# Kernel tuning notes

Hardware: AMD Instinct MI355X
Metric: run time of the kernel (lower is better)

Reference implementation:

```python
import jax, jax.numpy as jnp
import numpy as np
import math

D_MODEL = 512
N_HEADS = 8
FACTOR = 5
B, L = 2, 2048


def setup_inputs() -> dict:
    key = jax.random.key(0)
    ks = jax.random.split(key, 10)
    s = 1.0 / math.sqrt(D_MODEL)
    inp = {
        "x": jax.random.normal(ks[0], (B, L, D_MODEL), dtype=jnp.float32),
        "samp_idx": jax.random.randint(ks[1], (FACTOR * L,), 0, L),
        "Wq": jax.random.normal(ks[2], (D_MODEL, D_MODEL), dtype=jnp.float32) * s,
        "bq": jnp.zeros((D_MODEL,), dtype=jnp.float32),
        "Wk": jax.random.normal(ks[3], (D_MODEL, D_MODEL), dtype=jnp.float32) * s,
        "bk": jnp.zeros((D_MODEL,), dtype=jnp.float32),
        "Wv": jax.random.normal(ks[4], (D_MODEL, D_MODEL), dtype=jnp.float32) * s,
        "bv": jnp.zeros((D_MODEL,), dtype=jnp.float32),
        "Wo": jax.random.normal(ks[5], (D_MODEL, D_MODEL), dtype=jnp.float32) * s,
        "bo": jnp.zeros((D_MODEL,), dtype=jnp.float32),
    }
    return inp


def reference(x, Wq, bq, Wk, bk, Wv, bv, Wo, bo, samp_idx):
    B_, L_, D = x.shape
    H = N_HEADS
    dk = D // H
    scale = 1.0 / math.sqrt(dk)

    def proj(W, b):
        # torch Linear: x @ W.T + b, then split heads -> [B, H, L, dk]
        y = jnp.einsum('bld,ed->ble', x, W) + b
        return y.reshape(B_, L_, H, dk).transpose(0, 2, 1, 3)

    q = proj(Wq, bq)
    k = proj(Wk, bk)
    v = proj(Wv, bv)

    # _prob_QK: random key sampling (shared indices across B, H)
    K_sample = k[:, :, samp_idx, :]                       # [B, H, factor*L, dk]
    QKs = jnp.einsum('bhle,bhse->bhls', q, K_sample) * scale  # [B, H, L, factor*L]
    M = QKs.max(-1) - QKs.mean(-1)                        # [B, H, L]
    U = jnp.argmax(M, axis=-1)                            # [B, H] -- single query per head

    # gather the selected query per (b, h): [B, H, 1, dk]
    q_red = jnp.take_along_axis(q, U[:, :, None, None], axis=2)

    scores = jnp.einsum('bhle,bhse->bhls', q_red, k) * scale  # [B, H, 1, L]
    attn = jax.nn.softmax(scores, axis=-1)
    context = jnp.einsum('bhls,bhse->bhle', attn, v)          # [B, H, 1, dk]

    # expand to all query positions, merge heads
    context = jnp.broadcast_to(context, (B_, H, L_, dk))
    context = context.transpose(0, 2, 1, 3).reshape(B_, L_, D)
    return jnp.einsum('bld,ed->ble', context, Wo) + bo
```

## Files before the change

### kernel.cpp

```cpp
#include <hip/hip_runtime.h>

#define B_ 2
#define L_ 2048
#define D_ 512
#define H_ 8
#define DK 64
#define S_ 10240
#define SCALE 0.125f

#define QSZ (4096 * 512)

typedef _Float16 f16;
typedef __attribute__((ext_vector_type(8))) _Float16 f16x8;
typedef __attribute__((ext_vector_type(4))) float f32x4;

#define AS1 __attribute__((address_space(1)))
#define AS3 __attribute__((address_space(3)))

__global__ __launch_bounds__(256) void prep_kernel(
    const float* __restrict__ x,
    const float* __restrict__ Wq, const float* __restrict__ Wk,
    const float* __restrict__ bq, const float* __restrict__ bk,
    const int* __restrict__ samp,
    f16* __restrict__ xh, f16* __restrict__ xl,
    f16* __restrict__ wh, f16* __restrict__ wl,
    float* __restrict__ biascat, int* __restrict__ counts,
    float* __restrict__ xbc_part)
{
    const int bid = blockIdx.x;
    const int t = threadIdx.x;
    if (bid < 1024) {
        const size_t i0 = ((size_t)bid * 256 + t) * 8;
        const float4 a = *(const float4*)&x[i0];
        const float4 b = *(const float4*)&x[i0 + 4];
        const float vals[8] = {a.x, a.y, a.z, a.w, b.x, b.y, b.z, b.w};
        union { f16 h[8]; uint4 u; } H, Lo;
#pragma unroll
        for (int j = 0; j < 8; j++) {
            const f16 hh = (f16)vals[j];
            H.h[j] = hh;
            Lo.h[j] = (f16)(vals[j] - (float)hh);
        }
        *(uint4*)&xh[i0] = H.u;
        *(uint4*)&xl[i0] = Lo.u;
    } else if (bid < 1280) {
        const size_t i0 = ((size_t)(bid - 1024) * 256 + t) * 8;
        const float* src = (i0 < (size_t)512 * 512) ? Wq + i0
                                                    : Wk + (i0 - (size_t)512 * 512);
        const float4 a = *(const float4*)&src[0];
        const float4 b = *(const float4*)&src[4];
        const float vals[8] = {a.x, a.y, a.z, a.w, b.x, b.y, b.z, b.w};
        union { f16 h[8]; uint4 u; } H, Lo;
#pragma unroll
        for (int j = 0; j < 8; j++) {
            const f16 hh = (f16)vals[j];
            H.h[j] = hh;
            Lo.h[j] = (f16)(vals[j] - (float)hh);
        }
        *(uint4*)&wh[i0] = H.u;
        *(uint4*)&wl[i0] = Lo.u;
        if (bid == 1024)
            for (int e = t; e < 1024; e += 256)
                biascat[e] = (e < 512) ? bq[e] : bk[e - 512];
    } else if (bid < 1344) {
        const int p = bid - 1280;
        const int bb = p >> 5, chunk = p & 31;
        const int s0 = chunk * 320;
        float ax = 0.f, ay = 0.f;
        const float* xb = x + (size_t)bb * L_ * D_ + t * 2;
        for (int i = 0; i < 320; i++) {
            const int j = samp[s0 + i];
            const float2 v = *(const float2*)(xb + (size_t)j * D_);
            ax += v.x; ay += v.y;
        }
        float2 st; st.x = ax; st.y = ay;
        *(float2*)&xbc_part[((size_t)(bb * 32 + chunk)) * 512 + t * 2] = st;
    } else {
        int4 z; z.x = 0; z.y = 0; z.z = 0; z.w = 0;
        ((int4*)counts)[(bid - 1344) * 256 + t] = z;
    }
}

__global__ __launch_bounds__(256) void projqk_kernel(
    const f16* __restrict__ xh, const f16* __restrict__ xl,
    const f16* __restrict__ wh, const f16* __restrict__ wl,
    const float* __restrict__ biascat,
    const float* __restrict__ xbc_part, const float* __restrict__ Wk,
    const float* __restrict__ bk, const int* __restrict__ samp,
    int* __restrict__ counts, float* __restrict__ kbar,
    f16* __restrict__ qh, f16* __restrict__ ql,
    f16* __restrict__ kh, f16* __restrict__ kl)
{
    const int bid = blockIdx.x;
    const int t = threadIdx.x;

    __shared__ __align__(16) f16 lds[4 * 128 * 64];

    if (bid >= 256) {
        const int bh = bid - 256;
        const int b = bh >> 3, h = bh & 7;
        float* xc = (float*)lds;

        for (int i = bh * 640 + t; i < (bh + 1) * 640; i += 256)
            atomicAdd(&counts[samp[i]], 1);

        float ax = 0.f, ay = 0.f;
#pragma unroll
        for (int p = 0; p < 32; p++) {
            const float2 v = *(const float2*)&xbc_part[((size_t)(b * 32 + p)) * 512 + t * 2];
            ax += v.x; ay += v.y;
        }
        xc[t * 2]     = ax * (1.0f / (float)S_);
        xc[t * 2 + 1] = ay * (1.0f / (float)S_);
        __syncthreads();

        const int row = t >> 2, quarter = t & 3;
        const float* wr = Wk + (size_t)(h * 64 + row) * 512 + quarter * 128;
        float s = 0.f;
#pragma unroll 8
        for (int d = 0; d < 32; d++) {
            const float4 w4 = *(const float4*)&wr[d * 4];
            const int xo = quarter * 128 + d * 4;
            s += w4.x * xc[xo] + w4.y * xc[xo + 1] + w4.z * xc[xo + 2] + w4.w * xc[xo + 3];
        }
        s += __shfl_xor(s, 1);
        s += __shfl_xor(s, 2);
        if (quarter == 0) kbar[bh * 64 + row] = s + bk[h * 64 + row];
        return;
    }

    const int n0 = (bid & 31) * 128;
    const int e0 = (bid >> 5) * 128;

    f16* ash = lds;
    f16* asl = lds + 8192;
    f16* bsh = lds + 16384;
    f16* bsl = lds + 24576;

    const int lane = t & 63, wid = t >> 6;
    const int wr = wid >> 1, wc = wid & 1;
    const int lrow = lane & 15, lk = lane >> 4;
    const int srw = lane >> 3;
    const int scg = (lane & 7) ^ srw;

    f32x4 acc[4][4];
#pragma unroll
    for (int i = 0; i < 4; i++)
#pragma unroll
        for (int j = 0; j < 4; j++)
#pragma unroll
            for (int r = 0; r < 4; r++) acc[i][j][r] = 0.f;

    for (int kt = 0; kt < 8; kt++) {
        __syncthreads();
#pragma unroll
        for (int i_ = 0; i_ < 4; i_++) {
            const int chunk = wid * 4 + i_;
            const int row = chunk * 8 + srw;
            const size_t goa = (size_t)(n0 + row) * 512 + kt * 64 + scg * 8;
            const size_t gob = (size_t)(e0 + row) * 512 + kt * 64 + scg * 8;
            __builtin_amdgcn_global_load_lds((const AS1 void*)(xh + goa),
                                             (AS3 void*)(&ash[chunk * 512]), 16, 0, 0);
            __builtin_amdgcn_global_load_lds((const AS1 void*)(xl + goa),
                                             (AS3 void*)(&asl[chunk * 512]), 16, 0, 0);
            __builtin_amdgcn_global_load_lds((const AS1 void*)(wh + gob),
                                             (AS3 void*)(&bsh[chunk * 512]), 16, 0, 0);
            __builtin_amdgcn_global_load_lds((const AS1 void*)(wl + gob),
                                             (AS3 void*)(&bsl[chunk * 512]), 16, 0, 0);
        }
        __syncthreads();

#pragma unroll
        for (int kk = 0; kk < 2; kk++) {
            f16x8 ah[4], al[4], bh_[4], bl_[4];
#pragma unroll
            for (int lt = 0; lt < 4; lt++) {
                const int row = wr * 64 + lt * 16 + lrow;
                const int cs = (kk * 4 + lk) ^ (row & 7);
                const int o = row * 64 + cs * 8;
                ah[lt] = *(const f16x8*)&ash[o];
                al[lt] = *(const f16x8*)&asl[o];
            }
#pragma unroll
            for (int jt = 0; jt < 4; jt++) {
                const int row = wc * 64 + jt * 16 + lrow;
                const int cs = (kk * 4 + lk) ^ (row & 7);
                const int o = row * 64 + cs * 8;
                bh_[jt] = *(const f16x8*)&bsh[o];
                bl_[jt] = *(const f16x8*)&bsl[o];
            }
#pragma unroll
            for (int lt = 0; lt < 4; lt++)
#pragma unroll
                for (int jt = 0; jt < 4; jt++) {
                    acc[lt][jt] = __builtin_amdgcn_mfma_f32_16x16x32_f16(
                        ah[lt], bh_[jt], acc[lt][jt], 0, 0, 0);
                    acc[lt][jt] = __builtin_amdgcn_mfma_f32_16x16x32_f16(
                        ah[lt], bl_[jt], acc[lt][jt], 0, 0, 0);
                    acc[lt][jt] = __builtin_amdgcn_mfma_f32_16x16x32_f16(
                        al[lt], bh_[jt], acc[lt][jt], 0, 0, 0);
                }
        }
    }

    const int PSTR = 72;
    f16* tile = lds + wid * 64 * PSTR;
    const int ebase = e0 + wc * 64;
    const bool isQ = ((bid >> 5) < 4);
    const int colbase = ((bid >> 5) & 3) * 128;

#pragma unroll
    for (int round = 0; round < 2; round++) {
        __syncthreads();
#pragma unroll
        for (int jt = 0; jt < 4; jt++) {
            const float bval = biascat[ebase + jt * 16 + lrow];
#pragma unroll
            for (int lt = 0; lt < 4; lt++)
#pragma unroll
                for (int r = 0; r < 4; r++) {
                    const float y = acc[lt][jt][r] + bval;
                    const f16 hi = (f16)y;
                    const f16 val = (round == 0) ? hi : (f16)(y - (float)hi);
                    tile[(lt * 16 + lk * 4 + r) * PSTR + jt * 16 + lrow] = val;
                }
        }
        __syncthreads();
        f16* dst = isQ ? ((round == 0) ? qh : ql) : ((round == 0) ? kh : kl);
        for (int i = t; i < 2048; i += 256) {
            const int w = i >> 9, rem = i & 511, row = rem >> 3, c = rem & 7;
            const int n = n0 + (w >> 1) * 64 + row;
            const int col = colbase + (w & 1) * 64 + c * 8;
            *(uint4*)&dst[(size_t)n * 512 + col] =
                *(const uint4*)&lds[w * 64 * PSTR + row * PSTR + c * 8];
        }
    }
}

__global__ __launch_bounds__(256, 2) void mstat_kernel(
    const f16* __restrict__ qh, const f16* __restrict__ ql,
    const f16* __restrict__ kh, const f16* __restrict__ kl,
    const int* __restrict__ counts, const float* __restrict__ kbar,
    float* __restrict__ bestv, int* __restrict__ besti)
{
    const int id = blockIdx.x;
    const int xcd = id & 7, seq = id >> 3;
    const int bh = xcd * 2 + (seq >> 5);
    const int inner = seq & 31;
    const int lt16 = inner >> 1;
    const int js = inner & 1;
    const int jbase = js * 8;
    const int b = bh >> 3, h = bh & 7;
    const int l0 = lt16 * 128;
    const int t = threadIdx.x;
    const int lane = t & 63, wid = t >> 6;
    const int wr = wid >> 1, wc = wid & 1;
    const int lrow = lane & 15, lk = lane >> 4;

    __shared__ __align__(16) f16 kbuf[2][2][128 * 64];
    __shared__ float kbar_lds[64];
    __shared__ float dot_lds[128];
    __shared__ float wv_[4];
    __shared__ int wi_[4];

    f16x8 qa_h[2][4], qa_l[2][4];
    {
        const size_t qrowbase = (size_t)(b * L_ + l0 + wr * 64) * D_ + h * DK;
#pragma unroll
        for (int kk = 0; kk < 2; kk++)
#pragma unroll
            for (int lt = 0; lt < 4; lt++) {
                const size_t o = qrowbase + (size_t)(lt * 16 + lrow) * D_ + kk * 32 + lk * 8;
                qa_h[kk][lt] = *(const f16x8*)&qh[o];
                qa_l[kk][lt] = *(const f16x8*)&ql[o];
            }
    }
    if (t < 64) kbar_lds[t] = kbar[bh * 64 + t];

    const f16* khb = kh + (size_t)b * L_ * D_ + h * DK;
    const f16* klb = kl + (size_t)b * L_ * D_ + h * DK;

    const int srw = lane >> 3;
    const int scg = (lane & 7) ^ srw;
#define STAGE_TILE(jt, nb)                                                     \
    {                                                                          \
        const size_t gb0 = (size_t)((jt) * 128) * D_;                          \
        _Pragma("unroll")                                                      \
        for (int i_ = 0; i_ < 4; i_++) {                                       \
            const int chunk = wid * 4 + i_;                                    \
            const size_t go = gb0 + (size_t)(chunk * 8 + srw) * D_ + scg * 8;  \
            __builtin_amdgcn_global_load_lds(                                  \
                (const AS1 void*)(khb + go),                                   \
                (AS3 void*)(&kbuf[nb][0][chunk * 512]), 16, 0, 0);             \
            __builtin_amdgcn_global_load_lds(                                  \
                (const AS1 void*)(klb + go),                                   \
                (AS3 void*)(&kbuf[nb][1][chunk * 512]), 16, 0, 0);             \
        }                                                                      \
    }

    STAGE_TILE(jbase, 0)
    __syncthreads();

    float rmax[4][4];
#pragma unroll
    for (int lt = 0; lt < 4; lt++)
#pragma unroll
        for (int r = 0; r < 4; r++) rmax[lt][r] = -3.9e38f;

    int cur = 0;
    for (int jj = 0; jj < 8; jj++) {
        const int jt = jbase + jj;
        if (jj < 7) STAGE_TILE(jt + 1, cur ^ 1)

        f32x4 acc[4][4];
#pragma unroll
        for (int i = 0; i < 4; i++)
#pragma unroll
            for (int j = 0; j < 4; j++)
#pragma unroll
                for (int r = 0; r < 4; r++) acc[i][j][r] = 0.f;

#pragma unroll
        for (int kk = 0; kk < 2; kk++) {
            f16x8 bhf[4], blf[4];
#pragma unroll
            for (int jtt = 0; jtt < 4; jtt++) {
                const int row = wc * 64 + jtt * 16 + lrow;
                const int cs = (kk * 4 + lk) ^ (row & 7);
                const int o = row * 64 + cs * 8;
                bhf[jtt] = *(const f16x8*)&kbuf[cur][0][o];
                blf[jtt] = *(const f16x8*)&kbuf[cur][1][o];
            }
#pragma unroll
            for (int lt = 0; lt < 4; lt++)
#pragma unroll
                for (int jtt = 0; jtt < 4; jtt++) {
                    acc[lt][jtt] = __builtin_amdgcn_mfma_f32_16x16x32_f16(
                        qa_h[kk][lt], bhf[jtt], acc[lt][jtt], 0, 0, 0);
                    acc[lt][jtt] = __builtin_amdgcn_mfma_f32_16x16x32_f16(
                        qa_h[kk][lt], blf[jtt], acc[lt][jtt], 0, 0, 0);
                    acc[lt][jtt] = __builtin_amdgcn_mfma_f32_16x16x32_f16(
                        qa_l[kk][lt], bhf[jtt], acc[lt][jtt], 0, 0, 0);
                }
        }

#pragma unroll
        for (int jtt = 0; jtt < 4; jtt++) {
            const int cj = jt * 128 + wc * 64 + jtt * 16 + lrow;
            const float addend = (counts[cj] > 0) ? 0.f : -3.0e38f;
#pragma unroll
            for (int lt = 0; lt < 4; lt++)
#pragma unroll
                for (int r = 0; r < 4; r++)
                    rmax[lt][r] = fmaxf(rmax[lt][r], acc[lt][jtt][r] + addend);
        }

        __syncthreads();
        cur ^= 1;
    }

#pragma unroll
    for (int m = 1; m < 16; m <<= 1)
#pragma unroll
        for (int lt = 0; lt < 4; lt++)
#pragma unroll
            for (int r = 0; r < 4; r++)
                rmax[lt][r] = fmaxf(rmax[lt][r], __shfl_xor(rmax[lt][r], m));

    {
        float dlt[4];
#pragma unroll
        for (int lt = 0; lt < 4; lt++) {
            float d = 0.f;
#pragma unroll
            for (int kk = 0; kk < 2; kk++) {
                const f16x8 hv = qa_h[kk][lt];
                const f16x8 lv = qa_l[kk][lt];
#pragma unroll
                for (int i = 0; i < 8; i++)
                    d += ((float)hv[i] + (float)lv[i]) * kbar_lds[kk * 32 + lk * 8 + i];
            }
            dlt[lt] = d;
        }
#pragma unroll
        for (int lt = 0; lt < 4; lt++) {
            dlt[lt] += __shfl_xor(dlt[lt], 16);
            dlt[lt] += __shfl_xor(dlt[lt], 32);
        }
        if (lane < 16) {
#pragma unroll
            for (int lt = 0; lt < 4; lt++)
                dot_lds[wr * 64 + lt * 16 + lane] = dlt[lt];
        }
    }
    __syncthreads();

    float bv_ = -3.9e38f;
    int bi_ = 0x7fffffff;
#pragma unroll
    for (int lt = 0; lt < 4; lt++)
#pragma unroll
        for (int r = 0; r < 4; r++) {
            const int rl_ = wr * 64 + lt * 16 + lk * 4 + r;
            const float val = rmax[lt][r] - dot_lds[rl_];
            const int idx = l0 + rl_;
            if (val > bv_ || (val == bv_ && idx < bi_)) { bv_ = val; bi_ = idx; }
        }
#pragma unroll
    for (int m = 1; m < 64; m <<= 1) {
        const float ov = __shfl_xor(bv_, m);
        const int oi = __shfl_xor(bi_, m);
        if (ov > bv_ || (ov == bv_ && oi < bi_)) { bv_ = ov; bi_ = oi; }
    }
    if (lane == 0) { wv_[wid] = bv_; wi_[wid] = bi_; }
    __syncthreads();
    if (t == 0) {
        float fb = wv_[0]; int fi = wi_[0];
#pragma unroll
        for (int w = 1; w < 4; w++) {
            if (wv_[w] > fb || (wv_[w] == fb && wi_[w] < fi)) { fb = wv_[w]; fi = wi_[w]; }
        }
        bestv[bh * 32 + lt16 * 2 + js] = fb;
        besti[bh * 32 + lt16 * 2 + js] = fi;
    }
#undef STAGE_TILE
}

__global__ __launch_bounds__(256) void ctx_part_kernel(
    const f16* __restrict__ qh, const f16* __restrict__ ql,
    const f16* __restrict__ kh, const f16* __restrict__ kl,
    const float* __restrict__ x,
    const float* __restrict__ bestv, const int* __restrict__ besti,
    float* __restrict__ xbar_part, float* __restrict__ cm, float* __restrict__ cs)
{
    const int c = blockIdx.x;
    const int b = blockIdx.y;
    const int l0 = c * 16;
    const int t = threadIdx.x;

    __shared__ float qr[8][64];
    __shared__ float w[8][16];
    __shared__ int u_lds[8];

    if (t < 8) {
        const int bh = b * 8 + t;
        float best = -3.9e38f; int bi = 0x7fffffff;
        for (int cc = 0; cc < 32; cc++) {
            const float v = bestv[bh * 32 + cc];
            const int oi = besti[bh * 32 + cc];
            if (v > best || (v == best && oi < bi)) { best = v; bi = oi; }
        }
        u_lds[t] = bi;
    }
    __syncthreads();

    {
        const int h = t >> 5, i2 = (t & 31) * 2;
        const int u = u_lds[h];
        const size_t o = (size_t)(b * L_ + u) * D_ + h * DK + i2;
        qr[h][i2]     = (float)qh[o]     + (float)ql[o];
        qr[h][i2 + 1] = (float)qh[o + 1] + (float)ql[o + 1];
    }
    __syncthreads();

    {
        const int dotid = t >> 1, half = t & 1;
        const int row = dotid & 15, h = dotid >> 4;
        const size_t off = (size_t)(b * L_ + l0 + row) * D_ + h * DK + half * 32;
        const f16* krh = kh + off;
        const f16* krl = kl + off;
        float dot = 0.f;
#pragma unroll
        for (int cc = 0; cc < 4; cc++) {
            const f16x8 hv = *(const f16x8*)&krh[cc * 8];
            const f16x8 lv = *(const f16x8*)&krl[cc * 8];
#pragma unroll
            for (int i = 0; i < 8; i++)
                dot += ((float)hv[i] + (float)lv[i]) * qr[h][half * 32 + cc * 8 + i];
        }
        dot += __shfl_xor(dot, 1);
        if (half == 0) w[h][row] = dot * SCALE;
    }
    __syncthreads();

    if (t < 8) {
        float m = w[t][0];
#pragma unroll
        for (int i = 1; i < 16; i++) m = fmaxf(m, w[t][i]);
        float s = 0.f;
#pragma unroll
        for (int i = 0; i < 16; i++) {
            const float e = expf(w[t][i] - m);
            w[t][i] = e;
            s += e;
        }
        cm[(size_t)(b * 8 + t) * 128 + c] = m;
        cs[(size_t)(b * 8 + t) * 128 + c] = s;
    }
    __syncthreads();

    {
        float ax[8], ay[8];
#pragma unroll
        for (int h = 0; h < 8; h++) { ax[h] = 0.f; ay[h] = 0.f; }
        const float* xb = x + (size_t)(b * L_ + l0) * D_ + t * 2;
#pragma unroll
        for (int i = 0; i < 16; i++) {
            const float2 xv = *(const float2*)(xb + (size_t)i * D_);
#pragma unroll
            for (int h = 0; h < 8; h++) {
                ax[h] = fmaf(w[h][i], xv.x, ax[h]);
                ay[h] = fmaf(w[h][i], xv.y, ay[h]);
            }
        }
#pragma unroll
        for (int h = 0; h < 8; h++) {
            float2 st; st.x = ax[h]; st.y = ay[h];
            *(float2*)&xbar_part[((size_t)(b * 8 + h) * 128 + c) * 512 + t * 2] = st;
        }
    }
}

__global__ __launch_bounds__(256) void ctx_combine_kernel(
    const float* __restrict__ xbar_part, const float* __restrict__ cm,
    const float* __restrict__ cs, const float* __restrict__ Wv,
    const float* __restrict__ bv, float* __restrict__ ctx)
{
    const int bh = blockIdx.x;
    const int h = bh & 7;
    const int t = threadIdx.x;
    __shared__ float xbar[512];

    float M = -3.9e38f;
    for (int cc = 0; cc < 128; cc++) M = fmaxf(M, cm[(size_t)bh * 128 + cc]);
    float denom = 0.f, ax = 0.f, ay = 0.f;
    for (int cc = 0; cc < 128; cc++) {
        const float f = expf(cm[(size_t)bh * 128 + cc] - M);
        denom += f * cs[(size_t)bh * 128 + cc];
        const float2 p = *(const float2*)
            &xbar_part[((size_t)bh * 128 + cc) * 512 + t * 2];
        ax = fmaf(f, p.x, ax);
        ay = fmaf(f, p.y, ay);
    }
    xbar[t * 2] = ax; xbar[t * 2 + 1] = ay;
    __syncthreads();

    if (t < 64) {
        const float* wr = Wv + (size_t)(h * 64 + t) * D_;
        float acc = 0.f;
#pragma unroll 8
        for (int d = 0; d < 128; d++) {
            const float4 wv4 = *(const float4*)&wr[d * 4];
            acc += wv4.x * xbar[d * 4] + wv4.y * xbar[d * 4 + 1] +
                   wv4.z * xbar[d * 4 + 2] + wv4.w * xbar[d * 4 + 3];
        }
        ctx[bh * 64 + t] = acc / denom + bv[h * 64 + t];
    }
}

__global__ __launch_bounds__(256) void out_kernel(
    const float* __restrict__ ctx, const float* __restrict__ Wo,
    const float* __restrict__ bo, float* __restrict__ out)
{
    const int b = blockIdx.x;
    const int sl = blockIdx.y;
    const int t = threadIdx.x;
    __shared__ float cb[512];
    __shared__ float row[512];

    cb[t] = ctx[b * 512 + t];
    cb[t + 256] = ctx[b * 512 + 256 + t];
    __syncthreads();

#pragma unroll
    for (int r = 0; r < 2; r++) {
        const int e = t + r * 256;
        const float* wr = Wo + (size_t)e * D_;
        float acc = 0.f;
#pragma unroll 8
        for (int c = 0; c < 128; c++) {
            const float4 wv = *(const float4*)(wr + c * 4);
            acc += wv.x * cb[c * 4] + wv.y * cb[c * 4 + 1] +
                   wv.z * cb[c * 4 + 2] + wv.w * cb[c * 4 + 3];
        }
        row[e] = acc + bo[e];
    }
    __syncthreads();

    const float4* r4 = (const float4*)row;
    float4* o4 = (float4*)(out + ((size_t)b * L_ + sl * 32) * D_);
    for (int i = t; i < 32 * 128; i += 256) {
        const int l = i >> 7, c = i & 127;
        o4[l * 128 + c] = r4[c];
    }
}

extern "C" void kernel_launch(void* const* d_in, const int* in_sizes, int n_in,
                              void* d_out, int out_size, void* d_ws, size_t ws_size,
                              hipStream_t stream)
{
    const float* x   = (const float*)d_in[0];
    const int* samp  = (const int*)d_in[1];
    const float* Wq  = (const float*)d_in[2];
    const float* bq  = (const float*)d_in[3];
    const float* Wk  = (const float*)d_in[4];
    const float* bk  = (const float*)d_in[5];
    const float* Wv  = (const float*)d_in[6];
    const float* bv  = (const float*)d_in[7];
    const float* Wo  = (const float*)d_in[8];
    const float* bo  = (const float*)d_in[9];
    float* out = (float*)d_out;

    f16* qh = (f16*)d_ws;
    f16* ql = qh + QSZ;
    f16* kh = ql + QSZ;
    f16* kl = kh + QSZ;
    f16* xh = kl + QSZ;
    f16* xl = xh + QSZ;
    f16* wh = xl + QSZ;
    f16* wl = wh + 1024 * 512;
    float* fbase     = (float*)(wl + 1024 * 512);
    float* biascat   = fbase;
    float* xbc_part  = biascat + 1024;
    float* xbar_part = xbc_part + 32768;
    float* cm        = xbar_part + 1048576;
    float* cs        = cm + 2048;
    float* bestv     = cs + 2048;
    float* kbar      = bestv + 512;
    float* ctx       = kbar + 1024;
    int* counts      = (int*)(ctx + 1024);
    int* besti       = counts + 2048;

    prep_kernel<<<1346, 256, 0, stream>>>(x, Wq, Wk, bq, bk, samp,
                                          xh, xl, wh, wl, biascat, counts,
                                          xbc_part);
    projqk_kernel<<<272, 256, 0, stream>>>(xh, xl, wh, wl, biascat,
                                           xbc_part, Wk, bk, samp, counts, kbar,
                                           qh, ql, kh, kl);
    mstat_kernel<<<512, 256, 0, stream>>>(qh, ql, kh, kl, counts, kbar,
                                          bestv, besti);
    ctx_part_kernel<<<dim3(128, 2), 256, 0, stream>>>(qh, ql, kh, kl, x,
                                                      bestv, besti,
                                                      xbar_part, cm, cs);
    ctx_combine_kernel<<<16, 256, 0, stream>>>(xbar_part, cm, cs, Wv, bv, ctx);
    out_kernel<<<dim3(2, 64), 256, 0, stream>>>(ctx, Wo, bo, out);
}
```

Baseline: 145.0 us.

## Fuse ctx_part, ctx_combine and out kernels into one flag-synchronized tail kernel

```diff
diff --git a/kernel.cpp b/kernel.cpp
--- a/kernel.cpp
+++ b/kernel.cpp
@@ -25,7 +25,7 @@
     f16* __restrict__ xh, f16* __restrict__ xl,
     f16* __restrict__ wh, f16* __restrict__ wl,
     float* __restrict__ biascat, int* __restrict__ counts,
-    float* __restrict__ xbc_part)
+    float* __restrict__ xbc_part, int* __restrict__ flags)
 {
     const int bid = blockIdx.x;
     const int t = threadIdx.x;
@@ -78,6 +78,7 @@
     } else {
         int4 z; z.x = 0; z.y = 0; z.z = 0; z.w = 0;
         ((int4*)counts)[(bid - 1344) * 256 + t] = z;
+        if (bid == 1344 && t == 0) { flags[0] = 0; flags[1] = 0; }
     }
 }
 
@@ -426,172 +427,194 @@
 #undef STAGE_TILE
 }
 
-__global__ __launch_bounds__(256) void ctx_part_kernel(
+__global__ __launch_bounds__(256) void tail_kernel(
     const f16* __restrict__ qh, const f16* __restrict__ ql,
     const f16* __restrict__ kh, const f16* __restrict__ kl,
     const float* __restrict__ x,
     const float* __restrict__ bestv, const int* __restrict__ besti,
-    float* __restrict__ xbar_part, float* __restrict__ cm, float* __restrict__ cs)
+    const float* __restrict__ Wv, const float* __restrict__ bv,
+    const float* __restrict__ Wo, const float* __restrict__ bo,
+    float* __restrict__ xbar_part, float* __restrict__ cm,
+    float* __restrict__ cs, float* __restrict__ ctx,
+    float* __restrict__ out, int* __restrict__ flags)
 {
-    const int c = blockIdx.x;
-    const int b = blockIdx.y;
-    const int l0 = c * 16;
+    const int bid = blockIdx.x;
     const int t = threadIdx.x;
 
-    __shared__ float qr[8][64];
-    __shared__ float w[8][16];
-    __shared__ int u_lds[8];
-
-    if (t < 8) {
-        const int bh = b * 8 + t;
-        float best = -3.9e38f; int bi = 0x7fffffff;
-        for (int cc = 0; cc < 32; cc++) {
-            const float v = bestv[bh * 32 + cc];
-            const int oi = besti[bh * 32 + cc];
-            if (v > best || (v == best && oi < bi)) { best = v; bi = oi; }
-        }
-        u_lds[t] = bi;
-    }
-    __syncthreads();
-
-    {
-        const int h = t >> 5, i2 = (t & 31) * 2;
-        const int u = u_lds[h];
-        const size_t o = (size_t)(b * L_ + u) * D_ + h * DK + i2;
-        qr[h][i2]     = (float)qh[o]     + (float)ql[o];
-        qr[h][i2 + 1] = (float)qh[o + 1] + (float)ql[o + 1];
-    }
-    __syncthreads();
-
-    {
-        const int dotid = t >> 1, half = t & 1;
-        const int row = dotid & 15, h = dotid >> 4;
-        const size_t off = (size_t)(b * L_ + l0 + row) * D_ + h * DK + half * 32;
-        const f16* krh = kh + off;
-        const f16* krl = kl + off;
-        float dot = 0.f;
-#pragma unroll
-        for (int cc = 0; cc < 4; cc++) {
-            const f16x8 hv = *(const f16x8*)&krh[cc * 8];
-            const f16x8 lv = *(const f16x8*)&krl[cc * 8];
-#pragma unroll
-            for (int i = 0; i < 8; i++)
-                dot += ((float)hv[i] + (float)lv[i]) * qr[h][half * 32 + cc * 8 + i];
-        }
-        dot += __shfl_xor(dot, 1);
-        if (half == 0) w[h][row] = dot * SCALE;
-    }
-    __syncthreads();
-
-    if (t < 8) {
-        float m = w[t][0];
-#pragma unroll
-        for (int i = 1; i < 16; i++) m = fmaxf(m, w[t][i]);
-        float s = 0.f;
-#pragma unroll
-        for (int i = 0; i < 16; i++) {
-            const float e = expf(w[t][i] - m);
-            w[t][i] = e;
-            s += e;
-        }
-        cm[(size_t)(b * 8 + t) * 128 + c] = m;
-        cs[(size_t)(b * 8 + t) * 128 + c] = s;
-    }
-    __syncthreads();
-
-    {
-        float ax[8], ay[8];
-#pragma unroll
-        for (int h = 0; h < 8; h++) { ax[h] = 0.f; ay[h] = 0.f; }
-        const float* xb = x + (size_t)(b * L_ + l0) * D_ + t * 2;
-#pragma unroll
-        for (int i = 0; i < 16; i++) {
-            const float2 xv = *(const float2*)(xb + (size_t)i * D_);
+    if (bid < 256) {
+        const int c = bid & 127;
+        const int b = bid >> 7;
+        const int l0 = c * 16;
+
+        __shared__ float qr[8][64];
+        __shared__ float w[8][16];
+        __shared__ int u_lds[8];
+
+        if (t < 8) {
+            const int bh = b * 8 + t;
+            float best = -3.9e38f; int bi = 0x7fffffff;
+            for (int cc = 0; cc < 32; cc++) {
+                const float v = bestv[bh * 32 + cc];
+                const int oi = besti[bh * 32 + cc];
+                if (v > best || (v == best && oi < bi)) { best = v; bi = oi; }
+            }
+            u_lds[t] = bi;
+        }
+        __syncthreads();
+
+        {
+            const int h = t >> 5, i2 = (t & 31) * 2;
+            const int u = u_lds[h];
+            const size_t o = (size_t)(b * L_ + u) * D_ + h * DK + i2;
+            qr[h][i2]     = (float)qh[o]     + (float)ql[o];
+            qr[h][i2 + 1] = (float)qh[o + 1] + (float)ql[o + 1];
+        }
+        __syncthreads();
+
+        {
+            const int dotid = t >> 1, half = t & 1;
+            const int row = dotid & 15, h = dotid >> 4;
+            const size_t off = (size_t)(b * L_ + l0 + row) * D_ + h * DK + half * 32;
+            const f16* krh = kh + off;
+            const f16* krl = kl + off;
+            float dot = 0.f;
+#pragma unroll
+            for (int cc = 0; cc < 4; cc++) {
+                const f16x8 hv = *(const f16x8*)&krh[cc * 8];
+                const f16x8 lv = *(const f16x8*)&krl[cc * 8];
+#pragma unroll
+                for (int i = 0; i < 8; i++)
+                    dot += ((float)hv[i] + (float)lv[i]) * qr[h][half * 32 + cc * 8 + i];
+            }
+            dot += __shfl_xor(dot, 1);
+            if (half == 0) w[h][row] = dot * SCALE;
+        }
+        __syncthreads();
+
+        if (t < 8) {
+            float m = w[t][0];
+#pragma unroll
+            for (int i = 1; i < 16; i++) m = fmaxf(m, w[t][i]);
+            float s = 0.f;
+#pragma unroll
+            for (int i = 0; i < 16; i++) {
+                const float e = expf(w[t][i] - m);
+                w[t][i] = e;
+                s += e;
+            }
+            cm[(size_t)(b * 8 + t) * 128 + c] = m;
+            cs[(size_t)(b * 8 + t) * 128 + c] = s;
+        }
+        __syncthreads();
+
+        {
+            float ax[8], ay[8];
+#pragma unroll
+            for (int h = 0; h < 8; h++) { ax[h] = 0.f; ay[h] = 0.f; }
+            const float* xb = x + (size_t)(b * L_ + l0) * D_ + t * 2;
+#pragma unroll
+            for (int i = 0; i < 16; i++) {
+                const float2 xv = *(const float2*)(xb + (size_t)i * D_);
+#pragma unroll
+                for (int h = 0; h < 8; h++) {
+                    ax[h] = fmaf(w[h][i], xv.x, ax[h]);
+                    ay[h] = fmaf(w[h][i], xv.y, ay[h]);
+                }
+            }
 #pragma unroll
             for (int h = 0; h < 8; h++) {
-                ax[h] = fmaf(w[h][i], xv.x, ax[h]);
-                ay[h] = fmaf(w[h][i], xv.y, ay[h]);
-            }
-        }
-#pragma unroll
-        for (int h = 0; h < 8; h++) {
-            float2 st; st.x = ax[h]; st.y = ay[h];
-            *(float2*)&xbar_part[((size_t)(b * 8 + h) * 128 + c) * 512 + t * 2] = st;
-        }
-    }
-}
-
-__global__ __launch_bounds__(256) void ctx_combine_kernel(
-    const float* __restrict__ xbar_part, const float* __restrict__ cm,
-    const float* __restrict__ cs, const float* __restrict__ Wv,
-    const float* __restrict__ bv, float* __restrict__ ctx)
-{
-    const int bh = blockIdx.x;
-    const int h = bh & 7;
-    const int t = threadIdx.x;
-    __shared__ float xbar[512];
-
-    float M = -3.9e38f;
-    for (int cc = 0; cc < 128; cc++) M = fmaxf(M, cm[(size_t)bh * 128 + cc]);
-    float denom = 0.f, ax = 0.f, ay = 0.f;
-    for (int cc = 0; cc < 128; cc++) {
-        const float f = expf(cm[(size_t)bh * 128 + cc] - M);
-        denom += f * cs[(size_t)bh * 128 + cc];
-        const float2 p = *(const float2*)
-            &xbar_part[((size_t)bh * 128 + cc) * 512 + t * 2];
-        ax = fmaf(f, p.x, ax);
-        ay = fmaf(f, p.y, ay);
-    }
-    xbar[t * 2] = ax; xbar[t * 2 + 1] = ay;
-    __syncthreads();
-
-    if (t < 64) {
-        const float* wr = Wv + (size_t)(h * 64 + t) * D_;
-        float acc = 0.f;
+                float2 st; st.x = ax[h]; st.y = ay[h];
+                *(float2*)&xbar_part[((size_t)(b * 8 + h) * 128 + c) * 512 + t * 2] = st;
+            }
+        }
+
+        __threadfence();
+        __syncthreads();
+        if (t == 0)
+            __hip_atomic_fetch_add(&flags[0], 1, __ATOMIC_RELEASE,
+                                   __HIP_MEMORY_SCOPE_AGENT);
+    } else if (bid < 272) {
+        const int bh = bid - 256;
+        const int h = bh & 7;
+        __shared__ float xbar[512];
+
+        if (t == 0) {
+            while (__hip_atomic_load(&flags[0], __ATOMIC_ACQUIRE,
+                                     __HIP_MEMORY_SCOPE_AGENT) < 256)
+                __builtin_amdgcn_s_sleep(8);
+        }
+        __syncthreads();
+
+        float M = -3.9e38f;
+        for (int cc = 0; cc < 128; cc++) M = fmaxf(M, cm[(size_t)bh * 128 + cc]);
+        float denom = 0.f, ax = 0.f, ay = 0.f;
+        for (int cc = 0; cc < 128; cc++) {
+            const float f = expf(cm[(size_t)bh * 128 + cc] - M);
+            denom += f * cs[(size_t)bh * 128 + cc];
+            const float2 p = *(const float2*)
+                &xbar_part[((size_t)bh * 128 + cc) * 512 + t * 2];
+            ax = fmaf(f, p.x, ax);
+            ay = fmaf(f, p.y, ay);
+        }
+        xbar[t * 2] = ax; xbar[t * 2 + 1] = ay;
+        __syncthreads();
+
+        if (t < 64) {
+            const float* wr = Wv + (size_t)(h * 64 + t) * D_;
+            float acc = 0.f;
 #pragma unroll 8
-        for (int d = 0; d < 128; d++) {
-            const float4 wv4 = *(const float4*)&wr[d * 4];
-            acc += wv4.x * xbar[d * 4] + wv4.y * xbar[d * 4 + 1] +
-                   wv4.z * xbar[d * 4 + 2] + wv4.w * xbar[d * 4 + 3];
-        }
-        ctx[bh * 64 + t] = acc / denom + bv[h * 64 + t];
-    }
-}
-
-__global__ __launch_bounds__(256) void out_kernel(
-    const float* __restrict__ ctx, const float* __restrict__ Wo,
-    const float* __restrict__ bo, float* __restrict__ out)
-{
-    const int b = blockIdx.x;
-    const int sl = blockIdx.y;
-    const int t = threadIdx.x;
-    __shared__ float cb[512];
-    __shared__ float row[512];
-
-    cb[t] = ctx[b * 512 + t];
-    cb[t + 256] = ctx[b * 512 + 256 + t];
-    __syncthreads();
-
-#pragma unroll
-    for (int r = 0; r < 2; r++) {
-        const int e = t + r * 256;
-        const float* wr = Wo + (size_t)e * D_;
-        float acc = 0.f;
+            for (int d = 0; d < 128; d++) {
+                const float4 wv4 = *(const float4*)&wr[d * 4];
+                acc += wv4.x * xbar[d * 4] + wv4.y * xbar[d * 4 + 1] +
+                       wv4.z * xbar[d * 4 + 2] + wv4.w * xbar[d * 4 + 3];
+            }
+            ctx[bh * 64 + t] = acc / denom + bv[h * 64 + t];
+        }
+
+        __threadfence();
+        __syncthreads();
+        if (t == 0)
+            __hip_atomic_fetch_add(&flags[1], 1, __ATOMIC_RELEASE,
+                                   __HIP_MEMORY_SCOPE_AGENT);
+    } else {
+        const int idx = bid - 272;
+        const int b = idx >> 6;
+        const int sl = idx & 63;
+        __shared__ float cb[512];
+        __shared__ float row[512];
+
+        if (t == 0) {
+            while (__hip_atomic_load(&flags[1], __ATOMIC_ACQUIRE,
+                                     __HIP_MEMORY_SCOPE_AGENT) < 16)
+                __builtin_amdgcn_s_sleep(8);
+        }
+        __syncthreads();
+
+        cb[t] = ctx[b * 512 + t];
+        cb[t + 256] = ctx[b * 512 + 256 + t];
+        __syncthreads();
+
+#pragma unroll
+        for (int r = 0; r < 2; r++) {
+            const int e = t + r * 256;
+            const float* wr = Wo + (size_t)e * D_;
+            float acc = 0.f;
 #pragma unroll 8
-        for (int c = 0; c < 128; c++) {
-            const float4 wv = *(const float4*)(wr + c * 4);
-            acc += wv.x * cb[c * 4] + wv.y * cb[c * 4 + 1] +
-                   wv.z * cb[c * 4 + 2] + wv.w * cb[c * 4 + 3];
-        }
-        row[e] = acc + bo[e];
-    }
-    __syncthreads();
-
-    const float4* r4 = (const float4*)row;
-    float4* o4 = (float4*)(out + ((size_t)b * L_ + sl * 32) * D_);
-    for (int i = t; i < 32 * 128; i += 256) {
-        const int l = i >> 7, c = i & 127;
-        o4[l * 128 + c] = r4[c];
+            for (int c = 0; c < 128; c++) {
+                const float4 wv = *(const float4*)(wr + c * 4);
+                acc += wv.x * cb[c * 4] + wv.y * cb[c * 4 + 1] +
+                       wv.z * cb[c * 4 + 2] + wv.w * cb[c * 4 + 3];
+            }
+            row[e] = acc + bo[e];
+        }
+        __syncthreads();
+
+        const float4* r4 = (const float4*)row;
+        float4* o4 = (float4*)(out + ((size_t)b * L_ + sl * 32) * D_);
+        for (int i = t; i < 32 * 128; i += 256) {
+            const int l = i >> 7, c = i & 127;
+            o4[l * 128 + c] = r4[c];
+        }
     }
 }
 
@@ -630,18 +653,17 @@
     float* ctx       = kbar + 1024;
     int* counts      = (int*)(ctx + 1024);
     int* besti       = counts + 2048;
+    int* flags       = besti + 512;
 
     prep_kernel<<<1346, 256, 0, stream>>>(x, Wq, Wk, bq, bk, samp,
                                           xh, xl, wh, wl, biascat, counts,
-                                          xbc_part);
+                                          xbc_part, flags);
     projqk_kernel<<<272, 256, 0, stream>>>(xh, xl, wh, wl, biascat,
                                            xbc_part, Wk, bk, samp, counts, kbar,
                                            qh, ql, kh, kl);
     mstat_kernel<<<512, 256, 0, stream>>>(qh, ql, kh, kl, counts, kbar,
                                           bestv, besti);
-    ctx_part_kernel<<<dim3(128, 2), 256, 0, stream>>>(qh, ql, kh, kl, x,
-                                                      bestv, besti,
-                                                      xbar_part, cm, cs);
-    ctx_combine_kernel<<<16, 256, 0, stream>>>(xbar_part, cm, cs, Wv, bv, ctx);
-    out_kernel<<<dim3(2, 64), 256, 0, stream>>>(ctx, Wo, bo, out);
+    tail_kernel<<<400, 256, 0, stream>>>(qh, ql, kh, kl, x, bestv, besti,
+                                         Wv, bv, Wo, bo,
+                                         xbar_part, cm, cs, ctx, out, flags);
 }
```

Result: slower. 245.0 us (+69.0%).
